# Kernel tuning notes

Hardware: AMD Instinct MI355X
Metric: run time of the kernel (lower is better)

The kernel has to match this reference:

```python
import jax, jax.numpy as jnp
import numpy as np

N_ITER = 2
BIG = 1e16  # distance assigned to out-of-range superpixel neighbors (zero affinity)


def reference(x, stoken_size):
    B, C, H, W = x.shape
    sh = sw = int(stoken_size)
    nh, nw = H // sh, W // sw
    ns = nh * nw          # num_spixels
    P = H * W             # n_pixel

    pix = x.reshape(B, C, P)  # (B,C,P)
    # initial centroids: adaptive_avg_pool2d == block mean for divisible sizes
    spix = x.reshape(B, C, nh, sh, nw, sw).mean(axis=(3, 5)).reshape(B, C, ns)

    # init label map (nearest interpolation of the ns-label grid to HxW)
    ly = jnp.arange(H) // sh
    lx = jnp.arange(W) // sw
    init_label = (ly[:, None] * nw + lx[None, :]).reshape(-1)  # (P,)

    # 9-neighbor relative superpixel offsets
    rel = jnp.array([-nw - 1, -nw, -nw + 1, -1, 0, 1, nw - 1, nw, nw + 1])
    sidx = init_label[None, :] + rel[:, None]          # (9,P)
    valid = (sidx >= 0) & (sidx < ns)                  # same mask as get_abs_indices
    sidx_c = jnp.clip(sidx, 0, ns - 1)                 # safe gather index
    cols = jnp.broadcast_to(jnp.arange(P)[None, :], (9, P))
    bidx = jnp.broadcast_to(sidx_c[None], (B, 9, P))

    pn = (pix ** 2).sum(axis=1)   # (B,P)
    abs_aff = jnp.zeros((B, ns, P), x.dtype)
    for k in range(N_ITER):
        # pairwise squared distance pixel <-> 9 candidate superpixels
        sn = (spix ** 2).sum(axis=1)                        # (B,ns)
        dots = jnp.einsum('bcs,bcp->bsp', spix, pix)        # (B,ns,P)
        cross = jnp.take_along_axis(dots, bidx, axis=1)     # (B,9,P)
        sng = sn[:, sidx_c]                                 # (B,9,P)
        dist = pn[:, None, :] - 2.0 * cross + sng           # (B,9,P)
        dist = jnp.where(valid[None], dist, jnp.asarray(BIG, x.dtype))
        aff = jax.nn.softmax(-dist, axis=1) * valid[None]   # (B,9,P)
        # dense sparse-scatter: abs_aff[b, sidx[k,p], p] += aff[b,k,p]
        abs_aff = jnp.zeros((B, ns, P), x.dtype).at[:, sidx_c, cols].add(aff)
        if k < N_ITER - 1:
            num = jnp.einsum('bsp,bcp->bcs', abs_aff, pix)             # (B,C,ns)
            spix = num / (abs_aff.sum(axis=2)[:, None, :] + 1e-16)
    # entire ssn_iter runs under torch.no_grad in the original
    return (jax.lax.stop_gradient(abs_aff), ns)


def setup_inputs() -> dict:
    key = jax.random.key(0)
    x = jax.random.normal(key, (4, 64, 256, 256), dtype=jnp.float32)
    return {"x": x, "stoken_size": 16}
```

## Files before the change

kernel.cpp:

```cpp
#include <hip/hip_runtime.h>

#define BB 4
#define CCH 64
#define HH 256
#define WW 256
#define PP (HH*WW)
#define NS 256


__global__ __launch_bounds__(256) void kA_spix_init(const float* __restrict__ x,
                                                    float* __restrict__ spix) {
    int blk = blockIdx.x;
    int i = blk & 15;
    int c = (blk >> 4) & 63;
    int b = blk >> 10;
    int t = threadIdx.x;
    const float* base = x + ((size_t)(b*CCH + c))*PP + (size_t)i*16*WW + t;
    float s = 0.f;
    #pragma unroll
    for (int r = 0; r < 16; ++r) s += base[(size_t)r*WW];
    #pragma unroll
    for (int off = 8; off; off >>= 1) s += __shfl_down(s, off, 16);
    if ((t & 15) == 0) {
        int j = t >> 4;
        spix[((size_t)b*NS + (i*16 + j))*CCH + c] = s * (1.f/256.f);
    }
}

__global__ __launch_bounds__(256) void kF_fused(const float* __restrict__ x,
                                                const float* __restrict__ spix,
                                                float* __restrict__ partial,
                                                float* __restrict__ wpart) {
    __shared__ float sp[9][64];
    __shared__ float sn[9];
    __shared__ float affL[9][260];
    __shared__ float pixT[32][260];
    __shared__ float red[4][9][33];
    __shared__ float wsum[4][9];

    int blk = blockIdx.x;
    int l = blk & 255, b = blk >> 8;
    int by = l >> 4, bx = l & 15;
    int t = threadIdx.x;
    int lane = t & 63, w = t >> 6;

    for (int idx = t; idx < 9*64; idx += 256) {
        int k = idx >> 6, c = idx & 63;
        int rel = (k/3 - 1)*16 + (k % 3) - 1;
        int s = l + rel;
        float v = 0.f;
        if (s >= 0 && s < NS) v = spix[((size_t)b*NS + s)*CCH + c];
        sp[k][c] = v;
    }
    __syncthreads();
    if (t < 9) {
        float s = 0.f;
        #pragma unroll
        for (int c4 = 0; c4 < 16; ++c4) {
            float4 v = *reinterpret_cast<const float4*>(&sp[t][c4*4]);
            s += v.x*v.x + v.y*v.y + v.z*v.z + v.w*v.w;
        }
        sn[t] = s;
    }
    __syncthreads();

    int ty = t >> 4, tx = t & 15;
    int gp = (by*16 + ty)*WW + bx*16 + tx;
    const float* px = x + (size_t)b*CCH*PP + gp;

    float xr[64];
    float cross[9];
    #pragma unroll
    for (int k = 0; k < 9; ++k) cross[k] = 0.f;
    float pn = 0.f;
    #pragma unroll
    for (int cc = 0; cc < 16; ++cc) {
        float v0 = px[(size_t)(cc*4+0)*PP];
        float v1 = px[(size_t)(cc*4+1)*PP];
        float v2 = px[(size_t)(cc*4+2)*PP];
        float v3 = px[(size_t)(cc*4+3)*PP];
        xr[cc*4+0] = v0; xr[cc*4+1] = v1; xr[cc*4+2] = v2; xr[cc*4+3] = v3;
        pn += v0*v0 + v1*v1 + v2*v2 + v3*v3;
        #pragma unroll
        for (int k = 0; k < 9; ++k) {
            const float4 s = *reinterpret_cast<const float4*>(&sp[k][cc*4]);
            cross[k] += s.x*v0 + s.y*v1 + s.z*v2 + s.w*v3;
        }
    }

    float e[9];
    float m = -1e30f;
    #pragma unroll
    for (int k = 0; k < 9; ++k) {
        int rel = (k/3 - 1)*16 + (k % 3) - 1;
        int s = l + rel;
        bool valid = (s >= 0) && (s < NS);
        float z = -(pn - 2.f*cross[k] + sn[k]);
        e[k] = valid ? z : -3.0e38f;
        if (valid && z > m) m = z;
    }
    float sum = 0.f;
    #pragma unroll
    for (int k = 0; k < 9; ++k) {
        float v = (e[k] > -2.9e38f) ? expf(e[k] - m) : 0.f;
        e[k] = v;
        sum += v;
    }
    float inv = 1.f / sum;
    #pragma unroll
    for (int k = 0; k < 9; ++k) { e[k] *= inv; affL[k][t] = e[k]; }

    #pragma unroll
    for (int k = 0; k < 9; ++k) {
        float v = e[k];
        #pragma unroll
        for (int off = 32; off; off >>= 1) v += __shfl_xor(v, off);
        if (lane == 0) wsum[w][k] = v;
    }
    __syncthreads();
    if (t < 9) {
        wpart[((size_t)b*9 + t)*NS + l] =
            wsum[0][t] + wsum[1][t] + wsum[2][t] + wsum[3][t];
    }

    int cl = t & 31, q = t >> 5;
    #pragma unroll
    for (int half = 0; half < 2; ++half) {
        if (half) __syncthreads();
        #pragma unroll
        for (int ci = 0; ci < 32; ++ci) pixT[ci][t] = xr[half*32 + ci];
        __syncthreads();
        float acc[9];
        #pragma unroll
        for (int k = 0; k < 9; ++k) acc[k] = 0.f;
        #pragma unroll
        for (int i4 = 0; i4 < 8; ++i4) {
            int lp4 = q*32 + i4*4;
            const float4 v = *reinterpret_cast<const float4*>(&pixT[cl][lp4]);
            #pragma unroll
            for (int k = 0; k < 9; ++k) {
                const float4 a = *reinterpret_cast<const float4*>(&affL[k][lp4]);
                acc[k] += a.x*v.x + a.y*v.y + a.z*v.z + a.w*v.w;
            }
        }
        #pragma unroll
        for (int k = 0; k < 9; ++k) acc[k] += __shfl_down(acc[k], 32);
        if (lane < 32) {
            #pragma unroll
            for (int k = 0; k < 9; ++k) red[w][k][cl] = acc[k];
        }
        __syncthreads();
        for (int tt = t; tt < 9*32; tt += 256) {
            int k = tt >> 5, c2 = tt & 31;
            float s = red[0][k][c2] + red[1][k][c2] + red[2][k][c2] + red[3][k][c2];
            partial[(((size_t)b*9 + k)*NS + l)*CCH + half*32 + c2] = s;
        }
    }
}

__global__ __launch_bounds__(256) void kD_update(const float* __restrict__ partial,
                                                 const float* __restrict__ wpart,
                                                 float* __restrict__ spix) {
    int gid = blockIdx.x*256 + threadIdx.x;
    int c = gid & 63, s = (gid >> 6) & 255, b = gid >> 14;
    float num = 0.f, den = 0.f;
    #pragma unroll
    for (int k = 0; k < 9; ++k) {
        int rel = (k/3 - 1)*16 + (k%3 - 1);
        int l = s - rel;
        if (l >= 0 && l < NS) {
            num += partial[(((size_t)b*9 + k)*NS + l)*CCH + c];
            den += wpart[((size_t)b*9 + k)*NS + l];
        }
    }
    spix[((size_t)b*NS + s)*CCH + c] = num / (den + 1e-16f);
}

__global__ __launch_bounds__(256) void kBE(const float* __restrict__ x,
                                           const float* __restrict__ spix,
                                           float* __restrict__ out,
                                           int out_size) {
    __shared__ float spw[50][68];
    __shared__ float snw[50];
    __shared__ float affL[9][260];
    int blk = blockIdx.x;
    int y = blk & 255;
    int b = blk >> 8;
    int t = threadIdx.x;
    int ly = y >> 4;
    int base = ly*16 - 17;

    for (int idx = t; idx < 50*CCH; idx += 256) {
        int j = idx >> 6, c = idx & 63;
        int g = base + j;
        float v = 0.f;
        if (g >= 0 && g < NS) v = spix[((size_t)b*NS + g)*CCH + c];
        spw[j][c] = v;
    }
    __syncthreads();
    if (t < 50) {
        float s = 0.f;
        #pragma unroll
        for (int c4 = 0; c4 < 16; ++c4) {
            float4 v = *reinterpret_cast<const float4*>(&spw[t][c4*4]);
            s += v.x*v.x + v.y*v.y + v.z*v.z + v.w*v.w;
        }
        snw[t] = s;
    }
    __syncthreads();

    int p = y*WW + t;
    const float* px = x + (size_t)b*CCH*PP + p;
    int wl = 17 + (t >> 4);
    int nk[9];
    #pragma unroll
    for (int k = 0; k < 9; ++k) nk[k] = wl + (k/3 - 1)*16 + (k%3 - 1);

    float cross[9];
    #pragma unroll
    for (int k = 0; k < 9; ++k) cross[k] = 0.f;
    float pn = 0.f;
    #pragma unroll
    for (int cc = 0; cc < 16; ++cc) {
        float v0 = px[(size_t)(cc*4+0)*PP];
        float v1 = px[(size_t)(cc*4+1)*PP];
        float v2 = px[(size_t)(cc*4+2)*PP];
        float v3 = px[(size_t)(cc*4+3)*PP];
        pn += v0*v0 + v1*v1 + v2*v2 + v3*v3;
        #pragma unroll
        for (int k = 0; k < 9; ++k) {
            const float4 s = *reinterpret_cast<const float4*>(&spw[nk[k]][cc*4]);
            cross[k] += s.x*v0 + s.y*v1 + s.z*v2 + s.w*v3;
        }
    }

    int label = ly*16 + (t >> 4);
    float e[9];
    float m = -1e30f;
    #pragma unroll
    for (int k = 0; k < 9; ++k) {
        int rel = (k/3 - 1)*16 + (k%3 - 1);
        int sidx = label + rel;
        bool valid = (sidx >= 0) && (sidx < NS);
        float z = -(pn - 2.f*cross[k] + snw[nk[k]]);
        e[k] = valid ? z : -3.0e38f;
        if (valid && z > m) m = z;
    }
    float sum = 0.f;
    #pragma unroll
    for (int k = 0; k < 9; ++k) {
        float v = (e[k] > -2.9e38f) ? expf(e[k] - m) : 0.f;
        e[k] = v;
        sum += v;
    }
    float inv = 1.f / sum;
    #pragma unroll
    for (int k = 0; k < 9; ++k) affL[k][t] = e[k] * inv;
    __syncthreads();

    int w = t >> 6, lane = t & 63;
    int px4 = lane * 4;
    int labelbase = ly*16 + (px4 >> 4);
    float* orow = out + (size_t)b*NS*PP + (size_t)y*WW + px4;
    #pragma unroll 8
    for (int r = 0; r < 64; ++r) {
        int s = w + 4*r;
        int diff = s - labelbase + 17;
        float4 v = make_float4(0.f, 0.f, 0.f, 0.f);
        if ((unsigned)diff <= 34u && (diff & 15) < 3) {
            int k = (diff >> 4)*3 + (diff & 15);
            v = *(const float4*)&affL[k][px4];
        }
        *(float4*)(orow + (size_t)s*PP) = v;
    }
    if (blk == 0 && t == 0) out[out_size - 1] = 256.0f;
}

extern "C" void kernel_launch(void* const* d_in, const int* in_sizes, int n_in,
                              void* d_out, int out_size, void* d_ws, size_t ws_size,
                              hipStream_t stream) {
    (void)in_sizes; (void)n_in; (void)ws_size;
    const float* x = (const float*)d_in[0];
    float* out = (float*)d_out;
    float* ws = (float*)d_ws;

    float* spix    = ws;
    float* partial = spix + (size_t)BB*NS*CCH;
    float* wpart   = partial + (size_t)BB*9*NS*CCH;

    kA_spix_init<<<BB*CCH*16, 256, 0, stream>>>(x, spix);
    kF_fused<<<BB*NS, 256, 0, stream>>>(x, spix, partial, wpart);
    kD_update<<<BB*NS*CCH/256, 256, 0, stream>>>(partial, wpart, spix);
    kBE<<<BB*HH, 256, 0, stream>>>(x, spix, out, out_size);
}
```

Before: 116.6 us.

## Process two adjacent superpixels per block with 512 threads in fused assign kernel

The first-iteration fused kernel now handles a pair of horizontally adjacent superpixels per 512-thread block instead of one per 256-thread block. The 12 neighbouring centroids are shared between the two cells, and each row of 32 pixels is loaded contiguously, which gives wider coalesced reads. The channel reduction is redone in four 16-channel chunks with an extra shared-memory reduction stage. This cuts redundant centroid loads and improves memory access width, at the cost of more barriers and fewer blocks (512 in total).

```diff
diff --git a/kernel.cpp b/kernel.cpp
--- a/kernel.cpp
+++ b/kernel.cpp
@@ -27,45 +27,52 @@
     }
 }
 
-__global__ __launch_bounds__(256) void kF_fused(const float* __restrict__ x,
-                                                const float* __restrict__ spix,
-                                                float* __restrict__ partial,
-                                                float* __restrict__ wpart) {
-    __shared__ float sp[9][64];
-    __shared__ float sn[9];
-    __shared__ float affL[9][260];
-    __shared__ float pixT[32][260];
-    __shared__ float red[4][9][33];
-    __shared__ float wsum[4][9];
+__global__ __launch_bounds__(512, 4) void kF2(const float* __restrict__ x,
+                                              const float* __restrict__ spix,
+                                              float* __restrict__ partial,
+                                              float* __restrict__ wpart) {
+    __shared__ float wk[3][4][64];
+    __shared__ float sn[12];
+    __shared__ float affL[2][9][268];
+    __shared__ float pixT[2][16][268];
+    __shared__ float wsum[8][2][9];
+    float (*red)[9][17] = (float(*)[9][17])&pixT[0][0][0];
 
     int blk = blockIdx.x;
-    int l = blk & 255, b = blk >> 8;
-    int by = l >> 4, bx = l & 15;
+    int pair = blk & 127, b = blk >> 7;
+    int ly = pair >> 3, pi = pair & 7;
+    int l0 = ly*16 + pi*2;
+
     int t = threadIdx.x;
+    int r = t >> 5;
+    int c32 = t & 31;
+    int u = c32 >> 4;
+    int tt = r*16 + (c32 & 15);
     int lane = t & 63, w = t >> 6;
 
-    for (int idx = t; idx < 9*64; idx += 256) {
-        int k = idx >> 6, c = idx & 63;
-        int rel = (k/3 - 1)*16 + (k % 3) - 1;
-        int s = l + rel;
+    for (int idx = t; idx < 12*64; idx += 512) {
+        int j = idx >> 6, c = idx & 63;
+        int row = j >> 2, col = j & 3;
+        int base = (row == 0) ? -17 : (row == 1) ? -1 : 15;
+        int s = l0 + base + col;
         float v = 0.f;
         if (s >= 0 && s < NS) v = spix[((size_t)b*NS + s)*CCH + c];
-        sp[k][c] = v;
-    }
-    __syncthreads();
-    if (t < 9) {
+        wk[row][col][c] = v;
+    }
+    __syncthreads();
+    if (t < 12) {
+        int row = t >> 2, col = t & 3;
         float s = 0.f;
         #pragma unroll
         for (int c4 = 0; c4 < 16; ++c4) {
-            float4 v = *reinterpret_cast<const float4*>(&sp[t][c4*4]);
+            float4 v = *reinterpret_cast<const float4*>(&wk[row][col][c4*4]);
             s += v.x*v.x + v.y*v.y + v.z*v.z + v.w*v.w;
         }
         sn[t] = s;
     }
     __syncthreads();
 
-    int ty = t >> 4, tx = t & 15;
-    int gp = (by*16 + ty)*WW + bx*16 + tx;
+    int gp = (ly*16 + r)*WW + pi*32 + c32;
     const float* px = x + (size_t)b*CCH*PP + gp;
 
     float xr[64];
@@ -83,7 +90,7 @@
         pn += v0*v0 + v1*v1 + v2*v2 + v3*v3;
         #pragma unroll
         for (int k = 0; k < 9; ++k) {
-            const float4 s = *reinterpret_cast<const float4*>(&sp[k][cc*4]);
+            const float4 s = *reinterpret_cast<const float4*>(&wk[k/3][u + (k%3)][cc*4]);
             cross[k] += s.x*v0 + s.y*v1 + s.z*v2 + s.w*v3;
         }
     }
@@ -93,9 +100,9 @@
     #pragma unroll
     for (int k = 0; k < 9; ++k) {
         int rel = (k/3 - 1)*16 + (k % 3) - 1;
-        int s = l + rel;
+        int s = l0 + u + rel;
         bool valid = (s >= 0) && (s < NS);
-        float z = -(pn - 2.f*cross[k] + sn[k]);
+        float z = -(pn - 2.f*cross[k] + sn[(k/3)*4 + u + (k%3)]);
         e[k] = valid ? z : -3.0e38f;
         if (valid && z > m) m = z;
     }
@@ -108,52 +115,57 @@
     }
     float inv = 1.f / sum;
     #pragma unroll
-    for (int k = 0; k < 9; ++k) { e[k] *= inv; affL[k][t] = e[k]; }
+    for (int k = 0; k < 9; ++k) { e[k] *= inv; affL[u][k][tt] = e[k]; }
 
     #pragma unroll
     for (int k = 0; k < 9; ++k) {
         float v = e[k];
-        #pragma unroll
-        for (int off = 32; off; off >>= 1) v += __shfl_xor(v, off);
-        if (lane == 0) wsum[w][k] = v;
-    }
-    __syncthreads();
-    if (t < 9) {
-        wpart[((size_t)b*9 + t)*NS + l] =
-            wsum[0][t] + wsum[1][t] + wsum[2][t] + wsum[3][t];
-    }
-
-    int cl = t & 31, q = t >> 5;
-    #pragma unroll
-    for (int half = 0; half < 2; ++half) {
-        if (half) __syncthreads();
-        #pragma unroll
-        for (int ci = 0; ci < 32; ++ci) pixT[ci][t] = xr[half*32 + ci];
+        v += __shfl_xor(v, 1);  v += __shfl_xor(v, 2);
+        v += __shfl_xor(v, 4);  v += __shfl_xor(v, 8);
+        v += __shfl_xor(v, 32);
+        if ((lane & 15) == 0 && lane < 32) wsum[w][lane >> 4][k] = v;
+    }
+    __syncthreads();
+    if (t < 18) {
+        int u2 = t / 9, k = t % 9;
+        float s = 0.f;
+        #pragma unroll
+        for (int ww = 0; ww < 8; ++ww) s += wsum[ww][u2][k];
+        wpart[((size_t)b*9 + k)*NS + (l0 + u2)] = s;
+    }
+
+    int cl = t & 15, g = t >> 4;
+    int gu = g & 1, rr = g >> 1;
+    #pragma unroll
+    for (int ch = 0; ch < 4; ++ch) {
+        if (ch) __syncthreads();
+        #pragma unroll
+        for (int ci = 0; ci < 16; ++ci) pixT[u][ci][tt] = xr[ch*16 + ci];
         __syncthreads();
         float acc[9];
         #pragma unroll
         for (int k = 0; k < 9; ++k) acc[k] = 0.f;
         #pragma unroll
-        for (int i4 = 0; i4 < 8; ++i4) {
-            int lp4 = q*32 + i4*4;
-            const float4 v = *reinterpret_cast<const float4*>(&pixT[cl][lp4]);
+        for (int i4 = 0; i4 < 4; ++i4) {
+            int base = rr*16 + i4*4;
+            const float4 v = *reinterpret_cast<const float4*>(&pixT[gu][cl][base]);
             #pragma unroll
             for (int k = 0; k < 9; ++k) {
-                const float4 a = *reinterpret_cast<const float4*>(&affL[k][lp4]);
+                const float4 a = *reinterpret_cast<const float4*>(&affL[gu][k][base]);
                 acc[k] += a.x*v.x + a.y*v.y + a.z*v.z + a.w*v.w;
             }
         }
-        #pragma unroll
-        for (int k = 0; k < 9; ++k) acc[k] += __shfl_down(acc[k], 32);
-        if (lane < 32) {
+        __syncthreads();
+        #pragma unroll
+        for (int k = 0; k < 9; ++k) red[g][k][cl] = acc[k];
+        __syncthreads();
+        if (t < 288) {
+            int u2 = t / 144, rem = t % 144;
+            int k = rem >> 4, c2 = rem & 15;
+            float s = 0.f;
             #pragma unroll
-            for (int k = 0; k < 9; ++k) red[w][k][cl] = acc[k];
-        }
-        __syncthreads();
-        for (int tt = t; tt < 9*32; tt += 256) {
-            int k = tt >> 5, c2 = tt & 31;
-            float s = red[0][k][c2] + red[1][k][c2] + red[2][k][c2] + red[3][k][c2];
-            partial[(((size_t)b*9 + k)*NS + l)*CCH + half*32 + c2] = s;
+            for (int j = 0; j < 16; ++j) s += red[(j << 1) | u2][k][c2];
+            partial[(((size_t)b*9 + k)*NS + (l0 + u2))*CCH + ch*16 + c2] = s;
         }
     }
 }
@@ -289,7 +301,7 @@
     float* wpart   = partial + (size_t)BB*9*NS*CCH;
 
     kA_spix_init<<<BB*CCH*16, 256, 0, stream>>>(x, spix);
-    kF_fused<<<BB*NS, 256, 0, stream>>>(x, spix, partial, wpart);
+    kF2<<<BB*128, 512, 0, stream>>>(x, spix, partial, wpart);
     kD_update<<<BB*NS*CCH/256, 256, 0, stream>>>(partial, wpart, spix);
     kBE<<<BB*HH, 256, 0, stream>>>(x, spix, out, out_size);
 }
```

Measured after the change: 138.8 us. 19.0% more time.
